# Kernel tuning notes

Hardware: AMD Instinct MI355X
Metric: run time of the kernel (lower is better)

## Reference

```python
import jax, jax.numpy as jnp
import numpy as np

N_NODES = 100000
N_EDGES = 1600000
DIMS = [256, 128, 64, 1]  # decoder_dim=256, decoder_l=3 -> 256->128->64->1


def setup_inputs() -> dict:
    key = jax.random.key(0)
    ks = jax.random.split(key, 10)
    inp = {
        "b_z": jax.random.normal(ks[0], (N_NODES, DIMS[0]), jnp.float32),
        "src": jax.random.randint(ks[1], (N_EDGES,), 0, N_NODES, dtype=jnp.int64) if jax.config.jax_enable_x64 else jax.random.randint(ks[1], (N_EDGES,), 0, N_NODES),
        "dst": jax.random.randint(ks[2], (N_EDGES,), 0, N_NODES),
        "b_edge_weight": jax.random.uniform(ks[3], (N_EDGES,), jnp.float32),
        "b_size": 1000,
    }
    for i in range(3):
        inp[f"W{i+1}"] = jax.random.normal(ks[4 + i], (DIMS[i], DIMS[i + 1]), jnp.float32) / np.sqrt(DIMS[i]).astype(np.float32)
        inp[f"b{i+1}"] = jnp.zeros((DIMS[i + 1],), jnp.float32)
    return inp


def _gcn_layer(z, src, dst, ew, W, b, act):
    """DGL GraphConv, norm='both', weight=True, bias=True, in_feats > out_feats."""
    N = z.shape[0]
    ones = jnp.ones(src.shape[0], dtype=z.dtype)
    # unweighted structural degrees, clamped to >= 1 (DGL behavior)
    deg_out = jnp.clip(jax.ops.segment_sum(ones, src, num_segments=N), 1.0)
    deg_in = jnp.clip(jax.ops.segment_sum(ones, dst, num_segments=N), 1.0)
    norm_src = deg_out ** -0.5
    norm_dst = deg_in ** -0.5
    # src-normalize, then project (in > out so weight applied before aggregation)
    h = (z * norm_src[:, None]) @ W          # [N, out]
    m = h[src] * ew[:, None]                 # gather + edge weighting: [E, out]
    rst = jax.ops.segment_sum(m, dst, num_segments=N)  # scatter-sum to dst
    rst = rst * norm_dst[:, None] + b
    return act(rst) if act is not None else rst


def reference(b_z, src, dst, b_edge_weight, b_size, W1, b1, W2, b2, W3, b3):
    z = _gcn_layer(b_z, src, dst, b_edge_weight, W1, b1, jax.nn.relu)
    z = _gcn_layer(z, src, dst, b_edge_weight, W2, b2, jax.nn.relu)
    z = _gcn_layer(z, src, dst, b_edge_weight, W3, b3, None)  # last layer: no activation
    # nonlin_layers is empty (decoder_nonlin_out=None)
    return z.reshape(b_size, -1)
```

## Files before the change

### kernel.cpp

```cpp
#include <hip/hip_runtime.h>


constexpr int D0 = 256, D1 = 128, D2 = 64;
constexpr int NB = 1024;
constexpr int BSH = 7;
constexpr int EBLK = 4096;

typedef __attribute__((ext_vector_type(2))) float f32x2;
typedef __attribute__((ext_vector_type(4))) float f32x4;
typedef __attribute__((ext_vector_type(8))) short short8;

__device__ inline unsigned short f2bf(float f) {
  unsigned u = __builtin_bit_cast(unsigned, f);
  u += 0x7fffu + ((u >> 16) & 1u);
  return (unsigned short)(u >> 16);
}
__device__ inline float bf2f(unsigned short h) {
  unsigned u = ((unsigned)h) << 16;
  return __builtin_bit_cast(float, u);
}
__device__ inline int rdlane_i(int v, int l) { return __builtin_amdgcn_readlane(v, l); }
__device__ inline float rdlane_f(float v, int l) {
  return __builtin_bit_cast(float, __builtin_amdgcn_readlane(__builtin_bit_cast(int, v), l));
}

__global__ void k_chist2(const int* __restrict__ src, const int* __restrict__ dst,
                         int* __restrict__ bc_s, int* __restrict__ bc_d, int E) {
  __shared__ int hs[NB], hd[NB];
  for (int i = threadIdx.x; i < NB; i += 256) { hs[i] = 0; hd[i] = 0; }
  __syncthreads();
  int e0 = blockIdx.x * EBLK, e1 = min(e0 + EBLK, E);
  for (int i = e0 + threadIdx.x; i < e1; i += 256) {
    atomicAdd(&hs[src[i] >> BSH], 1);
    atomicAdd(&hd[dst[i] >> BSH], 1);
  }
  __syncthreads();
  for (int i = threadIdx.x; i < NB; i += 256) {
    bc_s[blockIdx.x * NB + i] = hs[i];
    bc_d[blockIdx.x * NB + i] = hd[i];
  }
}

__global__ void k_binscan(int* __restrict__ bc_s, int* __restrict__ bt_s,
                          int* __restrict__ bc_d, int* __restrict__ bt_d, int nbk) {
  __shared__ int ws[4];
  int* bc = blockIdx.y ? bc_d : bc_s;
  int* bt = blockIdx.y ? bt_d : bt_s;
  const int bin = blockIdx.x;
  const int t = threadIdx.x;
  const int chunk = (nbk + 255) / 256;
  const int b0 = t * chunk, b1 = min(b0 + chunk, nbk);
  int s = 0;
  for (int b = b0; b < b1; ++b) s += bc[b * NB + bin];
  int lane = t & 63, wid = t >> 6;
  int x = s;
#pragma unroll
  for (int d = 1; d < 64; d <<= 1) { int tt = __shfl_up(x, d); if (lane >= d) x += tt; }
  if (lane == 63) ws[wid] = x;
  __syncthreads();
  int wexcl = 0;
  for (int q = 0; q < wid; ++q) wexcl += ws[q];
  int run = wexcl + x - s;
  for (int b = b0; b < b1; ++b) {
    int v = bc[b * NB + bin];
    bc[b * NB + bin] = run;
    run += v;
  }
  if (t == 255) bt[bin] = run;
}

__global__ void k_btscan(const int* __restrict__ bt_s, int* __restrict__ cbase_s,
                         const int* __restrict__ bt_d, int* __restrict__ cbase_d,
                         int* __restrict__ offs_end, int E) {
  __shared__ int wsum[16];
  const int* bt = blockIdx.x ? bt_d : bt_s;
  int* cbase = blockIdx.x ? cbase_d : cbase_s;
  int tid = threadIdx.x, lane = tid & 63, wid = tid >> 6;
  int v = bt[tid];
  int x = v;
#pragma unroll
  for (int d = 1; d < 64; d <<= 1) { int t = __shfl_up(x, d); if (lane >= d) x += t; }
  if (lane == 63) wsum[wid] = x;
  __syncthreads();
  if (wid == 0 && lane < 16) {
    int s = wsum[lane];
#pragma unroll
    for (int d = 1; d < 16; d <<= 1) { int t = __shfl_up(s, d, 16); if (lane >= d) s += t; }
    wsum[lane] = s;
  }
  __syncthreads();
  int excl = x - v + (wid ? wsum[wid - 1] : 0);
  cbase[tid] = excl;
  if (tid == NB - 1) cbase[NB] = E;
  if (blockIdx.x == 1 && tid == 0) *offs_end = E;
}

__global__ void k_cpart2(const int* __restrict__ src, const int* __restrict__ dst,
                         const float* __restrict__ ew,
                         const int* __restrict__ bc_s, const int* __restrict__ cbase_s,
                         const int* __restrict__ bc_d, const int* __restrict__ cbase_d,
                         int* __restrict__ recs_s, int2* __restrict__ recs_d, int E) {
  __shared__ int cs[NB], cd[NB];
  for (int i = threadIdx.x; i < NB; i += 256) {
    cs[i] = cbase_s[i] + bc_s[blockIdx.x * NB + i];
    cd[i] = cbase_d[i] + bc_d[blockIdx.x * NB + i];
  }
  __syncthreads();
  int e0 = blockIdx.x * EBLK, e1 = min(e0 + EBLK, E);
  for (int i = e0 + threadIdx.x; i < e1; i += 256) {
    int s = src[i], d = dst[i];
    int ps = atomicAdd(&cs[s >> BSH], 1);
    recs_s[ps] = s;
    int pd = atomicAdd(&cd[d >> BSH], 1);
    recs_d[pd] = int2{s | ((d & 127) << 17), __builtin_bit_cast(int, ew[i])};
  }
}

__global__ void k_fine(const int2* __restrict__ recs, const int* __restrict__ cbase,
                       int2* __restrict__ esw, int* __restrict__ offs,
                       float* __restrict__ nd, int N) {
  __shared__ int h[128], cur[128];
  __shared__ int w0tot;
  int bin = blockIdx.x;
  int r0 = cbase[bin], r1 = cbase[bin + 1];
  int t = threadIdx.x;
  if (t < 128) h[t] = 0;
  __syncthreads();
  for (int i = r0 + t; i < r1; i += 256) atomicAdd(&h[recs[i].x >> 17], 1);
  __syncthreads();
  int v = 0, x = 0;
  if (t < 128) {
    v = h[t];
    x = v;
#pragma unroll
    for (int d = 1; d < 64; d <<= 1) { int tt = __shfl_up(x, d); if ((t & 63) >= d) x += tt; }
    if (t == 63) w0tot = x;
  }
  __syncthreads();
  if (t < 128) {
    int excl = x - v + (t >= 64 ? w0tot : 0);
    int node = bin * 128 + t;
    if (node < N) {
      offs[node] = r0 + excl;
      int d = v < 1 ? 1 : v;
      nd[node] = (float)(1.0 / sqrt((double)d));
    }
    cur[t] = r0 + excl;
  }
  __syncthreads();
  for (int i = r0 + t; i < r1; i += 256) {
    int2 rc = recs[i];
    int p = atomicAdd(&cur[rc.x >> 17], 1);
    esw[p] = int2{rc.x & 0x1ffff, rc.y};
  }
}

__global__ void k_fineh(const int* __restrict__ recs, const int* __restrict__ cbase,
                        float* __restrict__ ns, int N) {
  __shared__ int h[128];
  int bin = blockIdx.x;
  int r0 = cbase[bin], r1 = cbase[bin + 1];
  int t = threadIdx.x;
  if (t < 128) h[t] = 0;
  __syncthreads();
  for (int i = r0 + t; i < r1; i += 256) atomicAdd(&h[recs[i] & 127], 1);
  __syncthreads();
  if (t < 128) {
    int node = bin * 128 + t;
    if (node < N) {
      int d = h[t] < 1 ? 1 : h[t];
      ns[node] = (float)(1.0 / sqrt((double)d));
    }
  }
}

__global__ void k_wsplit(const float* __restrict__ W, short* __restrict__ hi,
                         short* __restrict__ lo, int K, int N) {
  int t = blockIdx.x * blockDim.x + threadIdx.x;
  if (t < K * N) {
    int k = t / N, n = t % N;
    float f = W[t];
    unsigned short h = f2bf(f);
    hi[(size_t)n * K + k] = (short)h;
    lo[(size_t)n * K + k] = (short)f2bf(f - bf2f(h));
  }
}

template <int K, int N, int WR, int WC>
__launch_bounds__(256, 2)
__global__ void k_gemm_mfma(const float* __restrict__ A, const float* __restrict__ ns,
                            const short* __restrict__ Wth, const short* __restrict__ Wtl,
                            float* __restrict__ C, int M) {
  constexpr int MR = 128 / WR / 16;
  constexpr int NC = N / WC / 16;
  __shared__ short8 Ah[4 * 128], Al[4 * 128];
  __shared__ short8 Bh[4 * N], Bl[4 * N];
  const int t = threadIdx.x;
  const int block_row = blockIdx.x * 128;
  const int lane = t & 63, wid = t >> 6;
  const int wr = wid / WC, wc = wid % WC;
  const int rowbase = wr * (128 / WR), colbase = wc * (N / WC);
  const int c = lane >> 4, lr = lane & 15;
  f32x4 acc[MR][NC] = {};
  const int r = t & 127;
  const int grow = block_row + r;
  float nsv = 0.f;
  if (t < 128 && grow < M) nsv = ns[grow];

  for (int k0 = 0; k0 < K; k0 += 32) {
    if (t < 128) {
      f32x4 v[8];
      if (grow < M) {
        const f32x4* ap = (const f32x4*)(A + (size_t)grow * K + k0);
#pragma unroll
        for (int i = 0; i < 8; ++i) v[i] = ap[i] * nsv;
      } else {
#pragma unroll
        for (int i = 0; i < 8; ++i) v[i] = f32x4{0.f, 0.f, 0.f, 0.f};
      }
#pragma unroll
      for (int cc = 0; cc < 4; ++cc) {
        short8 hi, lo;
#pragma unroll
        for (int i = 0; i < 8; ++i) {
          float f = v[cc * 2 + (i >> 2)][i & 3];
          unsigned short h = f2bf(f);
          hi[i] = (short)h;
          lo[i] = (short)f2bf(f - bf2f(h));
        }
        Ah[cc * 128 + r] = hi;
        Al[cc * 128 + r] = lo;
      }
    } else {
      const int tt = t - 128;
#pragma unroll
      for (int id = tt; id < N * 4; id += 128) {
        int col = id & (N - 1);
        int cb = id / N;
        Bh[cb * N + col] = *(const short8*)(Wth + (size_t)col * K + k0 + cb * 8);
        Bl[cb * N + col] = *(const short8*)(Wtl + (size_t)col * K + k0 + cb * 8);
      }
    }
    __syncthreads();
    short8 ah[MR], al[MR], bh[NC], bl[NC];
#pragma unroll
    for (int m = 0; m < MR; ++m) {
      int row = rowbase + m * 16 + lr;
      ah[m] = Ah[c * 128 + row];
      al[m] = Al[c * 128 + row];
    }
#pragma unroll
    for (int n = 0; n < NC; ++n) {
      int col = colbase + n * 16 + lr;
      bh[n] = Bh[c * N + col];
      bl[n] = Bl[c * N + col];
    }
#pragma unroll
    for (int m = 0; m < MR; ++m)
#pragma unroll
      for (int n = 0; n < NC; ++n) {
        acc[m][n] = __builtin_amdgcn_mfma_f32_16x16x32_bf16(ah[m], bh[n], acc[m][n], 0, 0, 0);
        acc[m][n] = __builtin_amdgcn_mfma_f32_16x16x32_bf16(ah[m], bl[n], acc[m][n], 0, 0, 0);
        acc[m][n] = __builtin_amdgcn_mfma_f32_16x16x32_bf16(al[m], bh[n], acc[m][n], 0, 0, 0);
      }
    __syncthreads();
  }
#pragma unroll
  for (int m = 0; m < MR; ++m) {
#pragma unroll
    for (int j = 0; j < 4; ++j) {
      int row = block_row + rowbase + m * 16 + (lane >> 4) * 4 + j;
      if (row < M) {
#pragma unroll
        for (int n = 0; n < NC; ++n)
          C[(size_t)row * N + colbase + n * 16 + lr] = acc[m][n][j];
      }
    }
  }
}

__launch_bounds__(256, 4)
__global__ void k_agg128f(const float* __restrict__ h, const int* __restrict__ offs,
                          const int2* __restrict__ esw, const float* __restrict__ nd,
                          const float* __restrict__ b1v, const float* __restrict__ ns,
                          const short* __restrict__ w2h, const short* __restrict__ w2l,
                          float* __restrict__ h2, int M) {
  __shared__ unsigned Ah32[16 * 64], Al32[16 * 64];
  const int t = threadIdx.x, lane = t & 63, wid = t >> 6;
  const int base = blockIdx.x * 16;
  const f32x2* hp = (const f32x2*)h;
  f32x2 bv = ((const f32x2*)b1v)[lane];
  for (int q = 0; q < 4; ++q) {
    const int row = wid * 4 + q;
    const int node = base + row;
    unsigned hi_pack = 0, lo_pack = 0;
    if (node < M) {
      int s0 = offs[node], s1 = offs[node + 1];
      float a0 = 0.f, a1 = 0.f;
      for (int bb = s0; bb < s1; bb += 64) {
        int kk = bb + lane;
        int sidx = 0;
        float wt = 0.f;
        if (kk < s1) {
          int2 e = esw[kk];
          sidx = e.x;
          wt = __builtin_bit_cast(float, e.y);
        }
        int cnt = min(64, s1 - bb);
        for (int jj = 0; jj < cnt; jj += 16) {
          f32x2 v[16];
          float wu[16];
#pragma unroll
          for (int u = 0; u < 16; ++u) {
            int s = rdlane_i(sidx, jj + u);
            wu[u] = rdlane_f(wt, jj + u);
            v[u] = hp[(size_t)(unsigned)s * 64 + lane];
          }
#pragma unroll
          for (int u = 0; u < 16; ++u) {
            a0 += v[u][0] * wu[u];
            a1 += v[u][1] * wu[u];
          }
        }
      }
      float ndv = nd[node], nsv = ns[node];
      float z0 = fmaxf(a0 * ndv + bv[0], 0.f) * nsv;
      float z1 = fmaxf(a1 * ndv + bv[1], 0.f) * nsv;
      unsigned short h0 = f2bf(z0), h1b = f2bf(z1);
      hi_pack = (unsigned)h0 | ((unsigned)h1b << 16);
      unsigned short l0 = f2bf(z0 - bf2f(h0)), l1 = f2bf(z1 - bf2f(h1b));
      lo_pack = (unsigned)l0 | ((unsigned)l1 << 16);
    }
    int idx = row * 64 + (lane ^ ((row & 7) << 2));
    Ah32[idx] = hi_pack;
    Al32[idx] = lo_pack;
  }
  __syncthreads();
  const int colB = wid * 16 + (lane & 15);
  const int koff = (lane >> 4) * 8;
  short8 bh[4], bl[4];
#pragma unroll
  for (int ks = 0; ks < 4; ++ks) {
    bh[ks] = *(const short8*)(w2h + (size_t)colB * 128 + ks * 32 + koff);
    bl[ks] = *(const short8*)(w2l + (size_t)colB * 128 + ks * 32 + koff);
  }
  const int arow = lane & 15, ac = lane >> 4;
  f32x4 acc = {};
#pragma unroll
  for (int ks = 0; ks < 4; ++ks) {
    int bidx = arow * 64 + ((ks * 16 + ac * 4) ^ ((arow & 7) << 2));
    short8 ah = *(const short8*)(Ah32 + bidx);
    short8 al = *(const short8*)(Al32 + bidx);
    acc = __builtin_amdgcn_mfma_f32_16x16x32_bf16(ah, bh[ks], acc, 0, 0, 0);
    acc = __builtin_amdgcn_mfma_f32_16x16x32_bf16(ah, bl[ks], acc, 0, 0, 0);
    acc = __builtin_amdgcn_mfma_f32_16x16x32_bf16(al, bh[ks], acc, 0, 0, 0);
  }
  const int crow = (lane >> 4) * 4;
  const int col = wid * 16 + (lane & 15);
#pragma unroll
  for (int j = 0; j < 4; ++j) {
    int node = base + crow + j;
    if (node < M) h2[(size_t)node * 64 + col] = acc[j];
  }
}

__global__ void k_agg64mv(const float* __restrict__ h, const int* __restrict__ offs,
                          const int2* __restrict__ esw, const float* __restrict__ nd,
                          const float* __restrict__ b2, const float* __restrict__ W3,
                          const float* __restrict__ ns, float* __restrict__ h3, int M) {
  int w = blockIdx.x * (blockDim.x >> 6) + (threadIdx.x >> 6);
  int lane = threadIdx.x & 63;
  if (w >= M) return;
  int s0 = offs[w], s1 = offs[w + 1];
  float acc = 0.f;
  for (int base = s0; base < s1; base += 64) {
    int kk = base + lane;
    int sidx = 0;
    float wt = 0.f;
    if (kk < s1) {
      int2 e = esw[kk];
      sidx = e.x;
      wt = __builtin_bit_cast(float, e.y);
    }
    int cnt = min(64, s1 - base);
    for (int jj = 0; jj < cnt; jj += 16) {
      float v[16], wu[16];
#pragma unroll
      for (int u = 0; u < 16; ++u) {
        int s = rdlane_i(sidx, jj + u);
        wu[u] = rdlane_f(wt, jj + u);
        v[u] = h[(size_t)(unsigned)s * 64 + lane];
      }
#pragma unroll
      for (int u = 0; u < 16; ++u) acc += v[u] * wu[u];
    }
  }
  float r = fmaxf(acc * nd[w] + b2[lane], 0.f);
  float p = r * W3[lane];
#pragma unroll
  for (int d = 32; d; d >>= 1) p += __shfl_xor(p, d);
  if (lane == 0) h3[w] = p * ns[w];
}

__global__ void k_aggfin(const float* __restrict__ h3, const int* __restrict__ offs,
                         const int2* __restrict__ esw, const float* __restrict__ nd,
                         const float* __restrict__ b3, float* __restrict__ out, int M) {
  int i = blockIdx.x * blockDim.x + threadIdx.x;
  if (i >= M) return;
  int s0 = offs[i], s1 = offs[i + 1];
  float acc = 0.f;
  int k = s0;
  for (; k + 4 <= s1; k += 4) {
    int2 e0 = esw[k], e1 = esw[k + 1], e2 = esw[k + 2], e3 = esw[k + 3];
    acc += h3[e0.x] * __builtin_bit_cast(float, e0.y)
         + h3[e1.x] * __builtin_bit_cast(float, e1.y)
         + h3[e2.x] * __builtin_bit_cast(float, e2.y)
         + h3[e3.x] * __builtin_bit_cast(float, e3.y);
  }
  for (; k < s1; ++k) {
    int2 e = esw[k];
    acc += h3[e.x] * __builtin_bit_cast(float, e.y);
  }
  out[i] = acc * nd[i] + b3[0];
}

extern "C" void kernel_launch(void* const* d_in, const int* in_sizes, int n_in,
                              void* d_out, int out_size, void* d_ws, size_t ws_size,
                              hipStream_t stream) {
  const float* b_z = (const float*)d_in[0];
  const int*   src = (const int*)d_in[1];
  const int*   dst = (const int*)d_in[2];
  const float* ew  = (const float*)d_in[3];
  const float* W1  = (const float*)d_in[5];
  const float* b1  = (const float*)d_in[6];
  const float* W2  = (const float*)d_in[7];
  const float* b2  = (const float*)d_in[8];
  const float* W3  = (const float*)d_in[9];
  const float* b3  = (const float*)d_in[10];
  const int N = in_sizes[0] / D0;
  const int E = in_sizes[1];
  float* out = (float*)d_out;

  char* ws = (char*)d_ws;
  size_t off_b = 0;
  auto alloc = [&](size_t bytes) -> void* {
    void* p = ws + off_b;
    off_b += (bytes + 255) & ~(size_t)255;
    return p;
  };
  const int nbk = (E + EBLK - 1) / EBLK;
  int*   bc_s    = (int*)alloc((size_t)nbk * NB * 4);
  int*   bc_d    = (int*)alloc((size_t)nbk * NB * 4);
  int*   bt_s    = (int*)alloc((size_t)NB * 4);
  int*   bt_d    = (int*)alloc((size_t)NB * 4);
  int*   cbase_s = (int*)alloc((size_t)(NB + 1) * 4);
  int*   cbase_d = (int*)alloc((size_t)(NB + 1) * 4);
  int*   offs    = (int*)alloc((size_t)(N + 1) * 4);
  int2*  esw     = (int2*)alloc((size_t)E * 8);
  float* nsrc    = (float*)alloc((size_t)N * 4);
  float* ndst    = (float*)alloc((size_t)N * 4);
  float* h1      = (float*)alloc((size_t)N * D1 * 4);
  float* h2      = (float*)alloc((size_t)N * D2 * 4);
  float* h3      = (float*)alloc((size_t)N * 4);
  short* wt1h    = (short*)alloc((size_t)D0 * D1 * 2);
  short* wt1l    = (short*)alloc((size_t)D0 * D1 * 2);
  short* wt2h    = (short*)alloc((size_t)D1 * D2 * 2);
  short* wt2l    = (short*)alloc((size_t)D1 * D2 * 2);
  int2*  recs_d = (int2*)h1;
  int*   recs_s = (int*)((char*)h1 + ((size_t)16 << 20));

  k_chist2<<<nbk, 256, 0, stream>>>(src, dst, bc_s, bc_d, E);
  k_binscan<<<dim3(NB, 2), 256, 0, stream>>>(bc_s, bt_s, bc_d, bt_d, nbk);
  k_btscan<<<2, 1024, 0, stream>>>(bt_s, cbase_s, bt_d, cbase_d, &offs[N], E);
  k_cpart2<<<nbk, 256, 0, stream>>>(src, dst, ew, bc_s, cbase_s, bc_d, cbase_d,
                                    recs_s, recs_d, E);
  k_fineh<<<NB, 256, 0, stream>>>(recs_s, cbase_s, nsrc, N);
  k_fine<<<NB, 256, 0, stream>>>(recs_d, cbase_d, esw, offs, ndst, N);

  k_wsplit<<<(D0 * D1 + 255) / 256, 256, 0, stream>>>(W1, wt1h, wt1l, D0, D1);
  k_wsplit<<<(D1 * D2 + 255) / 256, 256, 0, stream>>>(W2, wt2h, wt2l, D1, D2);

  k_gemm_mfma<D0, D1, 2, 2><<<(N + 127) / 128, 256, 0, stream>>>(b_z, nsrc, wt1h, wt1l, h1, N);
  k_agg128f<<<(N + 15) / 16, 256, 0, stream>>>(h1, offs, esw, ndst, b1, nsrc,
                                               wt2h, wt2l, h2, N);
  k_agg64mv<<<(N + 3) / 4, 256, 0, stream>>>(h2, offs, esw, ndst, b2, W3, nsrc, h3, N);
  k_aggfin<<<(N + 255) / 256, 256, 0, stream>>>(h3, offs, esw, ndst, b3, out, N);
}
```

Before: 332.9 us.

## Prefetch edge records across nodes in aggregation kernels and restructure bin scan

The bin-count scan now handles 16 bins per block, with coalesced column reads and a shared-memory partial prefix, instead of one bin per block. The layer-2 and layer-3 aggregation kernels load the four node offsets with a single vector read, prefetch the next node's edge records while the current node is processed, and defer the edge-weight readlane until after the gathers behind a scheduling barrier. k_agg64mv now processes four nodes per wave, so the grid shrinks. This is meant to hide edge-index load latency and cut scan launch overhead, at the cost of more registers and less parallelism per wave.

Result: no change. 328.3 us (-1.4%).

```diff
diff --git a/kernel.cpp b/kernel.cpp
--- a/kernel.cpp
+++ b/kernel.cpp
@@ -43,30 +43,27 @@
 
 __global__ void k_binscan(int* __restrict__ bc_s, int* __restrict__ bt_s,
                           int* __restrict__ bc_d, int* __restrict__ bt_d, int nbk) {
-  __shared__ int ws[4];
+  __shared__ int part[16][17];
   int* bc = blockIdx.y ? bc_d : bc_s;
   int* bt = blockIdx.y ? bt_d : bt_s;
-  const int bin = blockIdx.x;
-  const int t = threadIdx.x;
-  const int chunk = (nbk + 255) / 256;
-  const int b0 = t * chunk, b1 = min(b0 + chunk, nbk);
+  const int j = threadIdx.x & 15;
+  const int c = threadIdx.x >> 4;
+  const int bin = blockIdx.x * 16 + j;
+  const int chunk = (nbk + 15) / 16;
+  const int r0 = c * chunk, r1 = min(r0 + chunk, nbk);
   int s = 0;
-  for (int b = b0; b < b1; ++b) s += bc[b * NB + bin];
-  int lane = t & 63, wid = t >> 6;
-  int x = s;
-#pragma unroll
-  for (int d = 1; d < 64; d <<= 1) { int tt = __shfl_up(x, d); if (lane >= d) x += tt; }
-  if (lane == 63) ws[wid] = x;
-  __syncthreads();
-  int wexcl = 0;
-  for (int q = 0; q < wid; ++q) wexcl += ws[q];
-  int run = wexcl + x - s;
-  for (int b = b0; b < b1; ++b) {
+  for (int b = r0; b < r1; ++b) s += bc[b * NB + bin];
+  part[c][j] = s;
+  __syncthreads();
+  int pre = 0;
+  for (int q = 0; q < c; ++q) pre += part[q][j];
+  int run = pre;
+  for (int b = r0; b < r1; ++b) {
     int v = bc[b * NB + bin];
     bc[b * NB + bin] = run;
     run += v;
   }
-  if (t == 255) bt[bin] = run;
+  if (c == 15) bt[bin] = run;
 }
 
 __global__ void k_btscan(const int* __restrict__ bt_s, int* __restrict__ cbase_s,
@@ -288,38 +285,44 @@
   __shared__ unsigned Ah32[16 * 64], Al32[16 * 64];
   const int t = threadIdx.x, lane = t & 63, wid = t >> 6;
   const int base = blockIdx.x * 16;
+  const int nb0 = base + wid * 4;
   const f32x2* hp = (const f32x2*)h;
   f32x2 bv = ((const f32x2*)b1v)[lane];
+  int ov = offs[min(nb0 + min(lane, 5), M)];
+  int S0[4], S1[4];
+#pragma unroll
+  for (int q = 0; q < 4; ++q) { S0[q] = rdlane_i(ov, q); S1[q] = rdlane_i(ov, q + 1); }
+  int2 ecur{0, 0};
+  { int kk = S0[0] + lane; if (kk < S1[0]) ecur = esw[kk]; }
+#pragma unroll
   for (int q = 0; q < 4; ++q) {
     const int row = wid * 4 + q;
-    const int node = base + row;
+    const int node = nb0 + q;
+    int2 enxt{0, 0};
+    if (q < 3) { int kk = S0[q + 1] + lane; if (kk < S1[q + 1]) enxt = esw[kk]; }
     unsigned hi_pack = 0, lo_pack = 0;
     if (node < M) {
-      int s0 = offs[node], s1 = offs[node + 1];
+      const int s0 = S0[q], s1 = S1[q];
       float a0 = 0.f, a1 = 0.f;
+      int2 e = ecur;
       for (int bb = s0; bb < s1; bb += 64) {
-        int kk = bb + lane;
-        int sidx = 0;
-        float wt = 0.f;
-        if (kk < s1) {
-          int2 e = esw[kk];
-          sidx = e.x;
-          wt = __builtin_bit_cast(float, e.y);
-        }
+        if (bb != s0) { int kk = bb + lane; e = (kk < s1) ? esw[kk] : int2{0, 0}; }
+        int sidx = e.x;
+        float wt = __builtin_bit_cast(float, e.y);
         int cnt = min(64, s1 - bb);
         for (int jj = 0; jj < cnt; jj += 16) {
           f32x2 v[16];
-          float wu[16];
 #pragma unroll
           for (int u = 0; u < 16; ++u) {
             int s = rdlane_i(sidx, jj + u);
-            wu[u] = rdlane_f(wt, jj + u);
             v[u] = hp[(size_t)(unsigned)s * 64 + lane];
           }
+          __builtin_amdgcn_sched_barrier(0);
 #pragma unroll
           for (int u = 0; u < 16; ++u) {
-            a0 += v[u][0] * wu[u];
-            a1 += v[u][1] * wu[u];
+            float wu = rdlane_f(wt, jj + u);
+            a0 += v[u][0] * wu;
+            a1 += v[u][1] * wu;
           }
         }
       }
@@ -334,6 +337,7 @@
     int idx = row * 64 + (lane ^ ((row & 7) << 2));
     Ah32[idx] = hi_pack;
     Al32[idx] = lo_pack;
+    ecur = enxt;
   }
   __syncthreads();
   const int colB = wid * 16 + (lane & 15);
@@ -368,38 +372,51 @@
                           const int2* __restrict__ esw, const float* __restrict__ nd,
                           const float* __restrict__ b2, const float* __restrict__ W3,
                           const float* __restrict__ ns, float* __restrict__ h3, int M) {
-  int w = blockIdx.x * (blockDim.x >> 6) + (threadIdx.x >> 6);
-  int lane = threadIdx.x & 63;
-  if (w >= M) return;
-  int s0 = offs[w], s1 = offs[w + 1];
-  float acc = 0.f;
-  for (int base = s0; base < s1; base += 64) {
-    int kk = base + lane;
-    int sidx = 0;
-    float wt = 0.f;
-    if (kk < s1) {
-      int2 e = esw[kk];
-      sidx = e.x;
-      wt = __builtin_bit_cast(float, e.y);
-    }
-    int cnt = min(64, s1 - base);
-    for (int jj = 0; jj < cnt; jj += 16) {
-      float v[16], wu[16];
-#pragma unroll
-      for (int u = 0; u < 16; ++u) {
-        int s = rdlane_i(sidx, jj + u);
-        wu[u] = rdlane_f(wt, jj + u);
-        v[u] = h[(size_t)(unsigned)s * 64 + lane];
-      }
-#pragma unroll
-      for (int u = 0; u < 16; ++u) acc += v[u] * wu[u];
-    }
-  }
-  float r = fmaxf(acc * nd[w] + b2[lane], 0.f);
-  float p = r * W3[lane];
-#pragma unroll
-  for (int d = 32; d; d >>= 1) p += __shfl_xor(p, d);
-  if (lane == 0) h3[w] = p * ns[w];
+  const int lane = threadIdx.x & 63;
+  const int wave = blockIdx.x * (blockDim.x >> 6) + (threadIdx.x >> 6);
+  const int nb0 = wave * 4;
+  if (nb0 >= M) return;
+  int ov = offs[min(nb0 + min(lane, 5), M)];
+  int S0[4], S1[4];
+#pragma unroll
+  for (int q = 0; q < 4; ++q) { S0[q] = rdlane_i(ov, q); S1[q] = rdlane_i(ov, q + 1); }
+  float bv = b2[lane], w3 = W3[lane];
+  int2 ecur{0, 0};
+  { int kk = S0[0] + lane; if (kk < S1[0]) ecur = esw[kk]; }
+#pragma unroll
+  for (int q = 0; q < 4; ++q) {
+    const int node = nb0 + q;
+    int2 enxt{0, 0};
+    if (q < 3) { int kk = S0[q + 1] + lane; if (kk < S1[q + 1]) enxt = esw[kk]; }
+    if (node < M) {
+      const int s0 = S0[q], s1 = S1[q];
+      float acc = 0.f;
+      int2 e = ecur;
+      for (int bb = s0; bb < s1; bb += 64) {
+        if (bb != s0) { int kk = bb + lane; e = (kk < s1) ? esw[kk] : int2{0, 0}; }
+        int sidx = e.x;
+        float wt = __builtin_bit_cast(float, e.y);
+        int cnt = min(64, s1 - bb);
+        for (int jj = 0; jj < cnt; jj += 16) {
+          float v[16];
+#pragma unroll
+          for (int u = 0; u < 16; ++u) {
+            int s = rdlane_i(sidx, jj + u);
+            v[u] = h[(size_t)(unsigned)s * 64 + lane];
+          }
+          __builtin_amdgcn_sched_barrier(0);
+#pragma unroll
+          for (int u = 0; u < 16; ++u) acc += v[u] * rdlane_f(wt, jj + u);
+        }
+      }
+      float r = fmaxf(acc * nd[node] + bv, 0.f);
+      float p = r * w3;
+#pragma unroll
+      for (int d = 32; d; d >>= 1) p += __shfl_xor(p, d);
+      if (lane == 0) h3[node] = p * ns[node];
+    }
+    ecur = enxt;
+  }
 }
 
 __global__ void k_aggfin(const float* __restrict__ h3, const int* __restrict__ offs,
@@ -470,7 +487,7 @@
   int*   recs_s = (int*)((char*)h1 + ((size_t)16 << 20));
 
   k_chist2<<<nbk, 256, 0, stream>>>(src, dst, bc_s, bc_d, E);
-  k_binscan<<<dim3(NB, 2), 256, 0, stream>>>(bc_s, bt_s, bc_d, bt_d, nbk);
+  k_binscan<<<dim3(NB / 16, 2), 256, 0, stream>>>(bc_s, bt_s, bc_d, bt_d, nbk);
   k_btscan<<<2, 1024, 0, stream>>>(bt_s, cbase_s, bt_d, cbase_d, &offs[N], E);
   k_cpart2<<<nbk, 256, 0, stream>>>(src, dst, ew, bc_s, cbase_s, bc_d, cbase_d,
                                     recs_s, recs_d, E);
@@ -483,6 +500,6 @@
   k_gemm_mfma<D0, D1, 2, 2><<<(N + 127) / 128, 256, 0, stream>>>(b_z, nsrc, wt1h, wt1l, h1, N);
   k_agg128f<<<(N + 15) / 16, 256, 0, stream>>>(h1, offs, esw, ndst, b1, nsrc,
                                                wt2h, wt2l, h2, N);
-  k_agg64mv<<<(N + 3) / 4, 256, 0, stream>>>(h2, offs, esw, ndst, b2, W3, nsrc, h3, N);
+  k_agg64mv<<<(N + 15) / 16, 256, 0, stream>>>(h2, offs, esw, ndst, b2, W3, nsrc, h3, N);
   k_aggfin<<<(N + 255) / 256, 256, 0, stream>>>(h3, offs, esw, ndst, b3, out, N);
 }
```
